# Kernel tuning notes

Measured on AMD Instinct MI355X. Metric: run time of the kernel, lower is better.

## Reference

```python
import jax, jax.numpy as jnp
import numpy as np

B, DIM, L, H, W = 4, 128, 256, 8, 8
N = L * H * W
D_INNER, D_STATE, D_CONV, DT_RANK = 128, 8, 4, 8


def _ln(x, w, b, eps=1e-5):
    m = x.mean(-1, keepdims=True)
    v = ((x - m) ** 2).mean(-1, keepdims=True)
    return (x - m) * jax.lax.rsqrt(v + eps) * w + b


def _mamba_fusion(x, z_in, p, i):
    # x, z_in: (B, N, DIM). x drives the SSM; z_in provides the cross-modal gate.
    u = x @ p['Wx'][i]                                    # (B, N, D_INNER)
    z = z_in @ p['Wz'][i]                                 # (B, N, D_INNER)
    # causal depthwise conv1d along tokens, kernel D_CONV (torch pad=k-1 then truncate)
    up = jnp.pad(u, ((0, 0), (D_CONV - 1, 0), (0, 0)))
    w = p['conv_w'][i]                                    # (D_INNER, D_CONV)
    uc = sum(up[:, k:k + u.shape[1], :] * w[:, k] for k in range(D_CONV)) + p['conv_b'][i]
    uc = jax.nn.silu(uc)
    x_dbl = uc @ p['Wxproj'][i]                           # (B, N, DT_RANK + 2*D_STATE)
    dt_r, Bm, Cm = jnp.split(x_dbl, [DT_RANK, DT_RANK + D_STATE], axis=-1)
    dt = jax.nn.softplus(dt_r @ p['Wdt'][i] + p['bdt'][i])  # (B, N, D_INNER)
    A = -jnp.exp(p['A_log'][i])                           # (D_INNER, D_STATE)
    dA = jnp.exp(dt[..., None] * A)                       # (B, N, D_INNER, D_STATE)
    dBu = dt[..., None] * Bm[:, :, None, :] * uc[..., None]

    def step(h, inp):
        dA_t, dBu_t, C_t = inp
        h = dA_t * h + dBu_t                              # (B, D_INNER, D_STATE)
        return h, jnp.einsum('bds,bs->bd', h, C_t)

    h0 = jnp.zeros((u.shape[0], D_INNER, D_STATE), u.dtype)
    _, ys = jax.lax.scan(step, h0, (dA.swapaxes(0, 1), dBu.swapaxes(0, 1), Cm.swapaxes(0, 1)))
    y = ys.swapaxes(0, 1) + p['Dp'][i] * uc
    y = y * jax.nn.silu(z)
    return y @ p['Wout_m'][i] + p['bout_m'][i]


def _cross_block(in0, in1, p, i):
    skip = in0
    a = _ln(in0, p['ln0_w'][i], p['ln0_b'][i])
    b = _ln(in1, p['ln1_w'][i], p['ln1_b'][i])
    return skip + _mamba_fusion(a, b, p, i)


def setup_inputs() -> dict:
    key = jax.random.key(0)
    ks = jax.random.split(key, 16)
    s_in = 1.0 / np.sqrt(DIM)
    s_di = 1.0 / np.sqrt(D_INNER)
    inp = {
        'front': jax.random.normal(ks[0], (B, DIM, L, H, W), jnp.float32),
        'back': jax.random.normal(ks[1], (B, DIM, L, H, W), jnp.float32),
        'ln0_w': jnp.ones((2, DIM), jnp.float32),
        'ln0_b': jnp.zeros((2, DIM), jnp.float32),
        'ln1_w': jnp.ones((2, DIM), jnp.float32),
        'ln1_b': jnp.zeros((2, DIM), jnp.float32),
        'Wx': jax.random.normal(ks[2], (2, DIM, D_INNER), jnp.float32) * s_in,
        'Wz': jax.random.normal(ks[3], (2, DIM, D_INNER), jnp.float32) * s_in,
        'conv_w': jax.random.normal(ks[4], (2, D_INNER, D_CONV), jnp.float32) * 0.5,
        'conv_b': jnp.zeros((2, D_INNER), jnp.float32),
        'Wxproj': jax.random.normal(ks[5], (2, D_INNER, DT_RANK + 2 * D_STATE), jnp.float32) * s_di,
        'Wdt': jax.random.normal(ks[6], (2, DT_RANK, D_INNER), jnp.float32) * (1.0 / np.sqrt(DT_RANK)),
        'bdt': jnp.full((2, D_INNER), -4.6, jnp.float32),  # softplus^-1(~0.01)
        'A_log': jnp.broadcast_to(jnp.log(jnp.arange(1, D_STATE + 1, dtype=jnp.float32)), (2, D_INNER, D_STATE)).copy(),
        'Dp': jnp.ones((2, D_INNER), jnp.float32),
        'Wout_m': jax.random.normal(ks[7], (2, D_INNER, DIM), jnp.float32) * s_di,
        'bout_m': jnp.zeros((2, DIM), jnp.float32),
        'Wout': jax.random.normal(ks[8], (DIM, DIM), jnp.float32) * s_in,
        'bout': jnp.zeros((DIM,), jnp.float32),
    }
    return inp


def reference(front, back, ln0_w, ln0_b, ln1_w, ln1_b, Wx, Wz, conv_w, conv_b,
              Wxproj, Wdt, bdt, A_log, Dp, Wout_m, bout_m, Wout, bout):
    p = dict(ln0_w=ln0_w, ln0_b=ln0_b, ln1_w=ln1_w, ln1_b=ln1_b, Wx=Wx, Wz=Wz,
             conv_w=conv_w, conv_b=conv_b, Wxproj=Wxproj, Wdt=Wdt, bdt=bdt,
             A_log=A_log, Dp=Dp, Wout_m=Wout_m, bout_m=bout_m)
    ff = front.reshape(B, DIM, N).swapaxes(1, 2)          # (B, N, DIM)
    bf = back.reshape(B, DIM, N).swapaxes(1, 2)
    f_fus = _cross_block(ff, bf, p, 0)
    b_fus = _cross_block(bf, ff, p, 1)
    fusion = ((f_fus + b_fus) * 0.5) @ Wout + bout
    return fusion.swapaxes(1, 2).reshape(B, DIM, L, H, W)
```

## Files before the change

### kernel.cpp

```cpp
#include <hip/hip_runtime.h>

#define DEV static __device__ __forceinline__

typedef short s16x8 __attribute__((ext_vector_type(8)));
typedef float f32x4 __attribute__((ext_vector_type(4)));
typedef unsigned short u16;

DEV float b2f(u16 u){ return __uint_as_float(((unsigned int)u) << 16); }
DEV u16 f2b(float f){
  unsigned int x = __float_as_uint(f);
  x += 0x7fffu + ((x >> 16) & 1u);
  return (u16)(x >> 16);
}
DEV float silu_f(float x){ return x * __builtin_amdgcn_rcpf(1.f + __expf(-x)); }
DEV float softplus_f(float x){ return (x > 15.f) ? x : __logf(1.f + __expf(x)); }
DEV bool detf32(const void* lnw){ return *(const unsigned int*)lnw == 0x3F800000u; }
DEV float ldin(const void* p, long long i, bool f){
  return f ? ((const float*)p)[i] : b2f(((const u16*)p)[i]);
}

static constexpr int BATCH = 4;
static constexpr int NSEQ  = 16384;
static constexpr int RTOT  = BATCH * NSEQ;
static constexpr int GCH   = 256;
static constexpr int DIRSZ = BATCH*GCH*128*8;

DEV int swz(int row, int col){ return (row << 7) + (col ^ ((row & 7) << 3)); }

__global__ __launch_bounds__(256) void k_setup(
                        const void* ln0w, const void* ln0b, const void* ln1w, const void* ln1b,
                        const void* Wx, const void* Wz, const void* Wxp, const void* Wdt,
                        const void* bdt, const void* Alog, const void* convw, const void* convb,
                        const void* Dpr, const void* Woutm, const void* boutm,
                        const void* Wout, const void* bout,
                        u16* Wuz, u16* WdtBC, u16* Wcat, u16* WoutT,
                        float* buz, float* bdtf, float* bcat, float* boutf,
                        float* Aexp, float* convwF, float* convbF, float* DpF)
{
  bool f = detf32(ln0w);
  int tid = blockIdx.x * 256 + threadIdx.x;
  int gs  = gridDim.x * 256;
  for (int idx = tid; idx < 2*256*128; idx += gs){
    int d = idx >> 15; int n = (idx >> 7) & 255; int k = idx & 127;
    float wv;
    if (n < 128) wv = ldin(ln0w, d*128+k, f) * ldin(Wx, (long long)(d*128+k)*128 + n, f);
    else         wv = ldin(ln1w, (1-d)*128+k, f) * ldin(Wz, (long long)((1-d)*128+k)*128 + (n-128), f);
    Wuz[idx] = f2b(wv);
  }
  for (int idx = tid; idx < 2*256; idx += gs){
    int d = idx >> 8; int n = idx & 255;
    float s = 0.f;
    if (n < 128){
      for (int k = 0; k < 128; ++k)
        s += ldin(ln0b, d*128+k, f) * ldin(Wx, (long long)(d*128+k)*128 + n, f);
    } else {
      for (int k = 0; k < 128; ++k)
        s += ldin(ln1b, (1-d)*128+k, f) * ldin(Wz, (long long)((1-d)*128+k)*128 + (n-128), f);
    }
    buz[idx] = s;
  }
  for (int idx = tid; idx < 2*128; idx += gs)
    bdtf[idx] = ldin(bdt, idx, f);
  for (int idx = tid; idx < 2*144*128; idx += gs){
    int i = idx / (144*128); int rem = idx % (144*128); int n = rem >> 7; int k = rem & 127;
    if (n < 128){
      float s = 0.f;
      for (int j = 0; j < 8; ++j)
        s += ldin(Wxp, (long long)(i*128+k)*24 + j, f) * ldin(Wdt, (long long)(i*8+j)*128 + n, f);
      WdtBC[idx] = f2b(s);
    } else {
      WdtBC[idx] = f2b(ldin(Wxp, (long long)(i*128+k)*24 + (n - 120), f));
    }
  }
  for (int idx = tid; idx < 128*256; idx += gs){
    int n = idx >> 8; int k = idx & 255;
    Wcat[idx] = f2b(ldin(Woutm, (long long)k*128 + n, f));
  }
  for (int idx = tid; idx < 128*128; idx += gs){
    int n = idx >> 7, k = idx & 127;
    WoutT[idx] = f2b(ldin(Wout, (long long)k*128 + n, f));
  }
  for (int idx = tid; idx < 128; idx += gs){
    bcat[idx]  = ldin(boutm, idx, f) + ldin(boutm, 128 + idx, f);
    boutf[idx] = ldin(bout, idx, f);
  }
  for (int idx = tid; idx < 2*128*8; idx += gs)
    Aexp[idx] = -expf(ldin(Alog, idx, f));
  for (int idx = tid; idx < 2*128*4; idx += gs)
    convwF[idx] = ldin(convw, idx, f);
  for (int idx = tid; idx < 2*128; idx += gs){
    convbF[idx] = ldin(convb, idx, f);
    DpF[idx]   = ldin(Dpr, idx, f);
  }
}

__global__ __launch_bounds__(256) void k_ln(const void* front, const void* back, const void* ln0w,
                                            u16* xf, u16* xb, u16* sfbh)
{
  bool fF = detf32(ln0w);
  __shared__ u16 Af[64][130];
  __shared__ u16 Ab[64][130];
  __shared__ float Mf[64], Rf[64], Mb[64], Rb[64];
  int tid = threadIdx.x;
  long long r0 = (long long)blockIdx.x * 64;
  int b  = (int)(r0 >> 14);
  int n0 = (int)(r0 & 16383);
  if (fF){
    const float* fp = (const float*)front;
    const float* bp = (const float*)back;
    for (int it = 0; it < 8; ++it){
      int d = it*16 + (tid >> 4);
      int t = (tid & 15) * 4;
      long long gi = ((long long)(b*128 + d))*NSEQ + n0 + t;
      float4 vf = *(const float4*)&fp[gi];
      float4 vb = *(const float4*)&bp[gi];
      Af[t+0][d] = f2b(vf.x); Af[t+1][d] = f2b(vf.y);
      Af[t+2][d] = f2b(vf.z); Af[t+3][d] = f2b(vf.w);
      Ab[t+0][d] = f2b(vb.x); Ab[t+1][d] = f2b(vb.y);
      Ab[t+2][d] = f2b(vb.z); Ab[t+3][d] = f2b(vb.w);
    }
  } else {
    const u16* fp = (const u16*)front;
    const u16* bp = (const u16*)back;
    for (int it = 0; it < 4; ++it){
      int d = it*32 + (tid >> 3);
      int t = (tid & 7) * 8;
      long long gi = ((long long)(b*128 + d))*NSEQ + n0 + t;
      uint4 vf = *(const uint4*)&fp[gi];
      uint4 vb = *(const uint4*)&bp[gi];
      Af[t+0][d] = (u16)vf.x; Af[t+1][d] = (u16)(vf.x>>16);
      Af[t+2][d] = (u16)vf.y; Af[t+3][d] = (u16)(vf.y>>16);
      Af[t+4][d] = (u16)vf.z; Af[t+5][d] = (u16)(vf.z>>16);
      Af[t+6][d] = (u16)vf.w; Af[t+7][d] = (u16)(vf.w>>16);
      Ab[t+0][d] = (u16)vb.x; Ab[t+1][d] = (u16)(vb.x>>16);
      Ab[t+2][d] = (u16)vb.y; Ab[t+3][d] = (u16)(vb.y>>16);
      Ab[t+4][d] = (u16)vb.z; Ab[t+5][d] = (u16)(vb.z>>16);
      Ab[t+6][d] = (u16)vb.w; Ab[t+7][d] = (u16)(vb.w>>16);
    }
  }
  __syncthreads();
  {
    int t = tid >> 2, sub = tid & 3;
    float s = 0.f, ss = 0.f, s2 = 0.f, ss2 = 0.f;
    for (int k = 0; k < 32; ++k){
      float v = b2f(Af[t][sub*32 + k]); s  += v; ss  += v*v;
      float w = b2f(Ab[t][sub*32 + k]); s2 += w; ss2 += w*w;
    }
    for (int m = 1; m < 4; m <<= 1){
      s  += __shfl_xor(s,  m, 64); ss  += __shfl_xor(ss,  m, 64);
      s2 += __shfl_xor(s2, m, 64); ss2 += __shfl_xor(ss2, m, 64);
    }
    if (sub == 0){
      float mf = s  * (1.f/128.f); float vf = ss  * (1.f/128.f) - mf*mf;
      Mf[t] = mf; Rf[t] = rsqrtf(vf + 1e-5f);
      float mb = s2 * (1.f/128.f); float vb = ss2 * (1.f/128.f) - mb*mb;
      Mb[t] = mb; Rb[t] = rsqrtf(vb + 1e-5f);
    }
  }
  __syncthreads();
  for (int it = 0; it < 8; ++it){
    int t = it*8 + (tid >> 5);
    int c = (tid & 31) * 4;
    float mf = Mf[t], rf = Rf[t], mb = Mb[t], rb = Rb[t];
    float f0 = b2f(Af[t][c+0]), f1 = b2f(Af[t][c+1]), f2 = b2f(Af[t][c+2]), f3 = b2f(Af[t][c+3]);
    float g0 = b2f(Ab[t][c+0]), g1 = b2f(Ab[t][c+1]), g2 = b2f(Ab[t][c+2]), g3 = b2f(Ab[t][c+3]);
    ushort4 xo, zo, so;
    xo.x = f2b((f0-mf)*rf); xo.y = f2b((f1-mf)*rf); xo.z = f2b((f2-mf)*rf); xo.w = f2b((f3-mf)*rf);
    zo.x = f2b((g0-mb)*rb); zo.y = f2b((g1-mb)*rb); zo.z = f2b((g2-mb)*rb); zo.w = f2b((g3-mb)*rb);
    so.x = f2b(f0+g0); so.y = f2b(f1+g1); so.z = f2b(f2+g2); so.w = f2b(f3+g3);
    long long o = (r0 + t)*128 + c;
    *(ushort4*)&xf[o] = xo;
    *(ushort4*)&xb[o] = zo;
    *(ushort4*)&sfbh[o] = so;
  }
}

__global__ __launch_bounds__(256) void k_guz(const u16* __restrict__ xf,
                                             const u16* __restrict__ xb,
                                             const u16* __restrict__ Wuz,
                                             const float* __restrict__ buz,
                                             u16* __restrict__ u0, u16* __restrict__ u1,
                                             u16* __restrict__ z0, u16* __restrict__ z1)
{
  int dir = blockIdx.y;
  const u16* A = dir ? xb : xf;
  const u16* Wt = Wuz + dir*256*128;
  const float* bias = buz + dir*256;
  u16* outU = dir ? u1 : u0;
  u16* outZ = dir ? z0 : z1;
  __shared__ u16 Wl[256][72];
  __shared__ u16 Al[64][72];
  int tid = threadIdx.x;
  long long r0 = (long long)blockIdx.x * 64;
  int w = tid >> 6, lane = tid & 63;
  int q = lane >> 4, m = lane & 15;
  f32x4 acc[16];
  #pragma unroll
  for (int ct = 0; ct < 16; ++ct) acc[ct] = (f32x4){0.f,0.f,0.f,0.f};
  for (int kp = 0; kp < 2; ++kp){
    if (kp) __syncthreads();
    for (int ci = tid; ci < 256*8; ci += 256){
      int n = ci >> 3, c8 = ci & 7;
      *(uint4*)&Wl[n][c8*8] = *(const uint4*)&Wt[n*128 + kp*64 + c8*8];
    }
    for (int ci = tid; ci < 64*8; ci += 256){
      int rl = ci >> 3, c8 = ci & 7;
      *(uint4*)&Al[rl][c8*8] = *(const uint4*)&A[(r0 + rl)*128 + kp*64 + c8*8];
    }
    __syncthreads();
    #pragma unroll
    for (int kt = 0; kt < 2; ++kt){
      s16x8 af = *(const s16x8*)&Al[w*16 + m][kt*32 + q*8];
      #pragma unroll
      for (int ct = 0; ct < 16; ++ct){
        s16x8 bf = *(const s16x8*)&Wl[ct*16 + m][kt*32 + q*8];
        acc[ct] = __builtin_amdgcn_mfma_f32_16x16x32_bf16(af, bf, acc[ct], 0, 0, 0);
      }
    }
  }
  #pragma unroll
  for (int ct = 0; ct < 16; ++ct){
    int col = ct*16 + m;
    #pragma unroll
    for (int i = 0; i < 4; ++i){
      long long r = r0 + w*16 + q*4 + i;
      float v = acc[ct][i] + bias[col];
      if (col < 128) outU[r*128 + col] = f2b(v);
      else           outZ[r*128 + (col - 128)] = f2b(silu_f(v));
    }
  }
}

__global__ __launch_bounds__(256, 3) void k_cps(const u16* __restrict__ u0p,
                                             const u16* __restrict__ u1p,
                                             const float* __restrict__ convwF,
                                             const float* __restrict__ convbF,
                                             const u16* __restrict__ WdtBC,
                                             const float* __restrict__ bdtf,
                                             const float* __restrict__ Aexp,
                                             u16* __restrict__ uc0p, u16* __restrict__ uc1p,
                                             u16* __restrict__ yg,
                                             float* __restrict__ BCg,
                                             float* __restrict__ P, float* __restrict__ Q)
{
  __shared__ __align__(16) u16 AlF[64*128];
  __shared__ __align__(16) u16 WlF[144*128];
  int dir = blockIdx.y;
  const u16* u = dir ? u1p : u0p;
  u16* ucb = dir ? uc1p : uc0p;
  const u16* Wt = WdtBC + dir*18432;
  const float* bias = bdtf + dir*128;
  u16* dtb = yg + dir*128;
  float* BC = BCg + (long long)dir*RTOT*16;
  int tid = threadIdx.x;
  long long r0 = (long long)blockIdx.x * 64;
  int b  = (int)(r0 >> 14);
  int n0 = (int)(r0 & 16383);
  for (int ci = tid; ci < 144*16; ci += 256){
    int n = ci >> 4, c8 = ci & 15;
    *(uint4*)&WlF[(n << 7) + ((c8 ^ (n & 7)) << 3)] = *(const uint4*)&Wt[n*128 + c8*8];
  }
  {
    int c = tid & 127, h = tid >> 7;
    const float* wp = &convwF[(dir*128 + c)*4];
    float w0 = wp[0], w1 = wp[1], w2 = wp[2], w3 = wp[3];
    float cb = convbF[dir*128 + c];
    int t0 = h*32;
    const u16* up = u + (long long)b*NSEQ*128 + c;
    int nbase = n0 + t0;
    float win0 = (nbase-3 >= 0) ? b2f(up[(long long)(nbase-3)*128]) : 0.f;
    float win1 = (nbase-2 >= 0) ? b2f(up[(long long)(nbase-2)*128]) : 0.f;
    float win2 = (nbase-1 >= 0) ? b2f(up[(long long)(nbase-1)*128]) : 0.f;
    #pragma unroll
    for (int t = 0; t < 32; ++t){
      float cur = b2f(up[(long long)(nbase + t)*128]);
      float a = win0*w0 + win1*w1 + win2*w2 + cur*w3 + cb;
      u16 s = f2b(silu_f(a));
      AlF[swz(t0 + t, c)] = s;
      ucb[(r0 + t0 + t)*128 + c] = s;
      win0 = win1; win1 = win2; win2 = cur;
    }
  }
  __syncthreads();
  int w = tid >> 6, lane = tid & 63;
  int q = lane >> 4, m = lane & 15;
  f32x4 acc[9];
  #pragma unroll
  for (int ct = 0; ct < 9; ++ct) acc[ct] = (f32x4){0.f,0.f,0.f,0.f};
  #pragma unroll
  for (int kt = 0; kt < 4; ++kt){
    int sc = (kt*32 + q*8) ^ ((m & 7) << 3);
    s16x8 af = *(const s16x8*)&AlF[((w*16 + m) << 7) + sc];
    #pragma unroll
    for (int ct = 0; ct < 9; ++ct){
      s16x8 bf = *(const s16x8*)&WlF[((ct*16 + m) << 7) + sc];
      acc[ct] = __builtin_amdgcn_mfma_f32_16x16x32_bf16(af, bf, acc[ct], 0, 0, 0);
    }
  }
  __syncthreads();
  u16* Dl = WlF;
  float* BCl = (float*)&WlF[64*128];
  #pragma unroll
  for (int ct = 0; ct < 9; ++ct){
    int col = ct*16 + m;
    #pragma unroll
    for (int i = 0; i < 4; ++i){
      int rl = w*16 + q*4 + i;
      long long r = r0 + rl;
      float v = acc[ct][i];
      if (col < 128){
        u16 dv = f2b(softplus_f(v + bias[col]));
        dtb[r*256 + col] = dv;
        Dl[swz(rl, col)] = dv;
      } else {
        BC[r*16 + (col - 128)] = v;
        BCl[rl*16 + (col - 128)] = v;
      }
    }
  }
  __syncthreads();
  {
    int c = tid & 127, sh = tid >> 7;
    int g = (int)(r0 & 16383) >> 6;
    int base = sh*4;
    float Ac[4], Pr[4], H[4];
    bool fast = true;
    #pragma unroll
    for (int j = 0; j < 4; ++j){
      Ac[j] = Aexp[(dir*128 + c)*8 + base + j];
      fast = fast && (fabsf(Ac[j] + (float)(base + j + 1)) < 2e-4f);
      Pr[j] = 1.f; H[j] = 0.f;
    }
    if (fast){
      for (int t = 0; t < 64; ++t){
        int ce = swz(t, c);
        float d  = b2f(Dl[ce]);
        float uu = b2f(AlF[ce]);
        float du = d * uu;
        float E  = __expf(-d);
        float E2 = E*E, E3 = E2*E, E4 = E2*E2;
        float M  = base ? E4 : 1.f;
        float dA0 = M*E, dA1 = M*E2, dA2 = M*E3, dA3 = M*E4;
        H[0] = dA0*H[0] + du*BCl[t*16 + base+0]; Pr[0] *= dA0;
        H[1] = dA1*H[1] + du*BCl[t*16 + base+1]; Pr[1] *= dA1;
        H[2] = dA2*H[2] + du*BCl[t*16 + base+2]; Pr[2] *= dA2;
        H[3] = dA3*H[3] + du*BCl[t*16 + base+3]; Pr[3] *= dA3;
      }
    } else {
      for (int t = 0; t < 64; ++t){
        int ce = swz(t, c);
        float d  = b2f(Dl[ce]);
        float uu = b2f(AlF[ce]);
        float du = d * uu;
        #pragma unroll
        for (int j = 0; j < 4; ++j){
          float dA = __expf(d * Ac[j]);
          H[j]  = dA*H[j] + du*BCl[t*16 + base + j];
          Pr[j] *= dA;
        }
      }
    }
    long long o = (long long)dir*DIRSZ + (((long long)b*GCH + g)*128 + c)*8 + base;
    *(float4*)&P[o] = make_float4(Pr[0],Pr[1],Pr[2],Pr[3]);
    *(float4*)&Q[o] = make_float4(H[0],H[1],H[2],H[3]);
  }
}

__global__ __launch_bounds__(64) void k_scan2(const float* __restrict__ P,
                                              const float* __restrict__ Q,
                                              float* __restrict__ hinit)
{
  int idx = blockIdx.x*64 + threadIdx.x;
  int dir = idx >> 12;
  int rem = idx & 4095;
  int b  = rem >> 10;
  int cs = rem & 1023;
  long long base = (long long)dir*DIRSZ + (long long)b*GCH*1024 + cs;
  float h = 0.f;
  for (int g = 0; g < GCH; g += 8){
    long long o = base + (long long)g*1024;
    float p[8], qv[8];
    #pragma unroll
    for (int j = 0; j < 8; ++j){ p[j] = P[o + j*1024]; qv[j] = Q[o + j*1024]; }
    #pragma unroll
    for (int j = 0; j < 8; ++j){
      hinit[o + j*1024] = h;
      h = p[j]*h + qv[j];
    }
  }
}

__global__ __launch_bounds__(256) void k_scan3(const u16* __restrict__ uc0p,
                                               const u16* __restrict__ uc1p,
                                               const float* __restrict__ BCg,
                                               const float* __restrict__ hinit,
                                               const u16* __restrict__ z0p,
                                               const u16* __restrict__ z1p,
                                               const float* __restrict__ DpF,
                                               const float* __restrict__ Aexp,
                                               u16* yg)
{
  __shared__ float Bl[128][8];
  __shared__ float Cl[128][8];
  int dir = blockIdx.y;
  const u16* uc = dir ? uc1p : uc0p;
  const u16* zs = dir ? z1p : z0p;
  const float* BC = BCg + (long long)dir*RTOT*16;
  int tid = threadIdx.x;
  int gp = blockIdx.x & 127;
  int b  = blockIdx.x >> 7;
  long long tokbase = (long long)b*NSEQ + gp*128;
  for (int idx = tid; idx < 128*8; idx += 256){
    int row = idx >> 3, s = idx & 7;
    Bl[row][s] = BC[(tokbase + row)*16 + s];
    Cl[row][s] = BC[(tokbase + row)*16 + 8 + s];
  }
  __syncthreads();
  int c = tid & 127;
  int gh = tid >> 7;
  int g = gp*2 + gh;
  int doff = dir*128;
  float Ac[8], H[8];
  long long ho = (long long)dir*DIRSZ + (((long long)b*GCH + g)*128 + c)*8;
  float4 h0 = *(const float4*)&hinit[ho];
  float4 h1 = *(const float4*)&hinit[ho + 4];
  H[0]=h0.x; H[1]=h0.y; H[2]=h0.z; H[3]=h0.w;
  H[4]=h1.x; H[5]=h1.y; H[6]=h1.z; H[7]=h1.w;
  bool fast = true;
  #pragma unroll
  for (int s = 0; s < 8; ++s){
    Ac[s] = Aexp[(dir*128 + c)*8 + s];
    fast = fast && (fabsf(Ac[s] + (float)(s + 1)) < 2e-4f);
  }
  float dpc = DpF[dir*128 + c];
  long long rbase = (long long)b*NSEQ + g*64;
  if (fast){
    for (int t = 0; t < 64; ++t){
      long long r = rbase + t;
      float d  = b2f(yg[r*256 + doff + c]);
      float uu = b2f(uc[r*128 + c]);
      float du = d * uu;
      int rowl = gh*64 + t;
      float E  = __expf(-d);
      float E2 = E*E, E3 = E2*E, E4 = E2*E2;
      float dA[8] = {E, E2, E3, E4, E4*E, E4*E2, E4*E3, E4*E4};
      float y = 0.f;
      #pragma unroll
      for (int s = 0; s < 8; ++s){
        H[s] = dA[s]*H[s] + du*Bl[rowl][s];
        y += H[s]*Cl[rowl][s];
      }
      float zv = b2f(zs[r*128 + c]);
      yg[r*256 + doff + c] = f2b((y + dpc*uu) * zv);
    }
  } else {
    for (int t = 0; t < 64; ++t){
      long long r = rbase + t;
      float d  = b2f(yg[r*256 + doff + c]);
      float uu = b2f(uc[r*128 + c]);
      float du = d * uu;
      int rowl = gh*64 + t;
      float y = 0.f;
      #pragma unroll
      for (int s = 0; s < 8; ++s){
        float dA = __expf(d * Ac[s]);
        H[s] = dA*H[s] + du*Bl[rowl][s];
        y += H[s]*Cl[rowl][s];
      }
      float zv = b2f(zs[r*128 + c]);
      yg[r*256 + doff + c] = f2b((y + dpc*uu) * zv);
    }
  }
}

__global__ __launch_bounds__(256) void k_tail(const u16* __restrict__ yg,
                                              const u16* __restrict__ Wcat,
                                              const float* __restrict__ bcat,
                                              const u16* __restrict__ sfbh,
                                              const u16* __restrict__ WoutT,
                                              const float* __restrict__ boutf,
                                              void* outp, const void* dflag)
{
  __shared__ u16 Wl[128][136];
  __shared__ u16 Al[64][136];
  __shared__ u16 Sl[64][136];
  int tid = threadIdx.x;
  long long r0 = (long long)blockIdx.x * 64;
  int w = tid >> 6, lane = tid & 63;
  int q = lane >> 4, m = lane & 15;
  f32x4 acc[8];
  #pragma unroll
  for (int ct = 0; ct < 8; ++ct) acc[ct] = (f32x4){0.f,0.f,0.f,0.f};
  for (int kp = 0; kp < 2; ++kp){
    if (kp) __syncthreads();
    for (int ci = tid; ci < 128*16; ci += 256){
      int n = ci >> 4, c8 = ci & 15;
      *(uint4*)&Wl[n][c8*8] = *(const uint4*)&Wcat[n*256 + kp*128 + c8*8];
    }
    for (int ci = tid; ci < 64*16; ci += 256){
      int rl = ci >> 4, c8 = ci & 15;
      *(uint4*)&Al[rl][c8*8] = *(const uint4*)&yg[(r0 + rl)*256 + kp*128 + c8*8];
    }
    __syncthreads();
    #pragma unroll
    for (int kt = 0; kt < 4; ++kt){
      s16x8 af = *(const s16x8*)&Al[w*16 + m][kt*32 + q*8];
      #pragma unroll
      for (int ct = 0; ct < 8; ++ct){
        s16x8 bf = *(const s16x8*)&Wl[ct*16 + m][kt*32 + q*8];
        acc[ct] = __builtin_amdgcn_mfma_f32_16x16x32_bf16(af, bf, acc[ct], 0, 0, 0);
      }
    }
  }
  #pragma unroll
  for (int ct = 0; ct < 8; ++ct){
    int col = ct*16 + m;
    #pragma unroll
    for (int i = 0; i < 4; ++i){
      int rl = w*16 + q*4 + i;
      long long r = r0 + rl;
      Sl[rl][col] = f2b(acc[ct][i] + bcat[col] + b2f(sfbh[r*128 + col]));
    }
  }
  __syncthreads();
  for (int ci = tid; ci < 128*16; ci += 256){
    int n = ci >> 4, c8 = ci & 15;
    *(uint4*)&Wl[n][c8*8] = *(const uint4*)&WoutT[n*128 + c8*8];
  }
  __syncthreads();
  f32x4 acc2[8];
  #pragma unroll
  for (int ct = 0; ct < 8; ++ct) acc2[ct] = (f32x4){0.f,0.f,0.f,0.f};
  #pragma unroll
  for (int kt = 0; kt < 4; ++kt){
    s16x8 af = *(const s16x8*)&Sl[w*16 + m][kt*32 + q*8];
    #pragma unroll
    for (int ct = 0; ct < 8; ++ct){
      s16x8 bf = *(const s16x8*)&Wl[ct*16 + m][kt*32 + q*8];
      acc2[ct] = __builtin_amdgcn_mfma_f32_16x16x32_bf16(af, bf, acc2[ct], 0, 0, 0);
    }
  }
  u16* Tl = &Al[0][0];
  #pragma unroll
  for (int ct = 0; ct < 8; ++ct){
    int col = ct*16 + m;
    #pragma unroll
    for (int i = 0; i < 4; ++i){
      int rl = w*16 + q*4 + i;
      Tl[col*68 + rl] = f2b(0.5f*acc2[ct][i] + boutf[col]);
    }
  }
  __syncthreads();
  long long b = r0 >> 14; long long tok0 = r0 & 16383;
  bool fo = detf32(dflag);
  if (fo){
    float* of = (float*)outp;
    for (int idx = tid; idx < 128*16; idx += 256){
      int n = idx >> 4; int t0 = (idx & 15)*4;
      float4 v;
      v.x = b2f(Tl[n*68 + t0+0]); v.y = b2f(Tl[n*68 + t0+1]);
      v.z = b2f(Tl[n*68 + t0+2]); v.w = b2f(Tl[n*68 + t0+3]);
      *(float4*)&of[(((long long)(b*128 + n)) << 14) + tok0 + t0] = v;
    }
  } else {
    u16* ob = (u16*)outp;
    for (int idx = tid; idx < 128*16; idx += 256){
      int n = idx >> 4; int t0 = (idx & 15)*4;
      ushort4 v;
      v.x = Tl[n*68 + t0+0]; v.y = Tl[n*68 + t0+1];
      v.z = Tl[n*68 + t0+2]; v.w = Tl[n*68 + t0+3];
      *(ushort4*)&ob[(((long long)(b*128 + n)) << 14) + tok0 + t0] = v;
    }
  }
}

extern "C" void kernel_launch(void* const* d_in, const int* in_sizes, int n_in,
                              void* d_out, int out_size, void* d_ws, size_t ws_size,
                              hipStream_t stream)
{
  (void)in_sizes; (void)n_in; (void)out_size; (void)ws_size;
  const void* front = d_in[0];
  const void* back  = d_in[1];
  const void* ln0w  = d_in[2];
  const void* ln0b  = d_in[3];
  const void* ln1w  = d_in[4];
  const void* ln1b  = d_in[5];
  const void* Wx    = d_in[6];
  const void* Wz    = d_in[7];
  const void* convw = d_in[8];
  const void* convb = d_in[9];
  const void* Wxp   = d_in[10];
  const void* Wdt   = d_in[11];
  const void* bdt   = d_in[12];
  const void* Alog  = d_in[13];
  const void* Dpr   = d_in[14];
  const void* Woutm = d_in[15];
  const void* boutm = d_in[16];
  const void* Wout  = d_in[17];
  const void* bout  = d_in[18];

  char* p = (char*)d_ws;
  auto alloc = [&](size_t bytes) -> void* {
    void* q = (void*)p; p += (bytes + 255) & ~(size_t)255; return q;
  };
  u16*   xf    = (u16*)  alloc((size_t)RTOT*128*2);
  u16*   xb    = (u16*)  alloc((size_t)RTOT*128*2);
  u16*   sfbh  = (u16*)  alloc((size_t)RTOT*128*2);
  u16*   u0    = (u16*)  alloc((size_t)RTOT*128*2);
  u16*   u1    = (u16*)  alloc((size_t)RTOT*128*2);
  u16*   z0    = (u16*)  alloc((size_t)RTOT*128*2);
  u16*   z1    = (u16*)  alloc((size_t)RTOT*128*2);
  float* BC    = (float*)alloc((size_t)2*RTOT*16*4);
  float* Pb    = (float*)alloc((size_t)2*DIRSZ*4);
  float* Qb    = (float*)alloc((size_t)2*DIRSZ*4);
  float* hin   = (float*)alloc((size_t)2*DIRSZ*4);
  u16*   yg    = (u16*)  alloc((size_t)RTOT*256*2);
  u16*   Wuz   = (u16*)  alloc(2*256*128*2);
  u16*   WdtBC = (u16*)  alloc(2*144*128*2);
  u16*   Wcat  = (u16*)  alloc(128*256*2);
  u16*   WoutT = (u16*)  alloc(128*128*2);
  float* buz   = (float*)alloc(2*256*4);
  float* bdtf  = (float*)alloc(2*128*4);
  float* bcat  = (float*)alloc(128*4);
  float* boutf = (float*)alloc(128*4);
  float* Aexp  = (float*)alloc(2*128*8*4);
  float* convwF= (float*)alloc(2*128*4*4);
  float* convbF= (float*)alloc(2*128*4);
  float* DpF   = (float*)alloc(2*128*4);

  k_setup<<<128,256,0,stream>>>(ln0w,ln0b,ln1w,ln1b,Wx,Wz,Wxp,Wdt,bdt,Alog,convw,convb,Dpr,
                                Woutm,boutm,Wout,bout,
                                Wuz,WdtBC,Wcat,WoutT,buz,bdtf,bcat,boutf,Aexp,
                                convwF,convbF,DpF);
  k_ln<<<RTOT/64,256,0,stream>>>(front,back,ln0w,xf,xb,sfbh);

  dim3 g2(RTOT/64, 2);
  k_guz<<<g2,256,0,stream>>>(xf, xb, Wuz, buz, u0, u1, z0, z1);
  k_cps<<<g2,256,0,stream>>>(u0, u1, convwF, convbF, WdtBC, bdtf, Aexp,
                             xf, xb, yg, BC, Pb, Qb);
  k_scan2<<<128,64,0,stream>>>(Pb, Qb, hin);
  dim3 g3(BATCH*GCH/2, 2);
  k_scan3<<<g3,256,0,stream>>>(xf, xb, BC, hin, z0, z1, DpF, Aexp, yg);
  k_tail<<<RTOT/64,256,0,stream>>>(yg, Wcat, bcat, sfbh, WoutT, boutf, d_out, ln0w);
}
```

Measured before the change: 329.4 us.

## Swizzle k_guz LDS, simplify chunk-scan decay products, trim k_tail LDS

k_guz drops its padded shared tiles for XOR-swizzled 64-wide rows to avoid bank conflicts and asks for 4 blocks per CU. In the chunk scan, the running decay product is no longer multiplied every step. It is recomputed once from the sum of dt, the fast path splits by state half with vectorized B loads, and the generic path uses exp(sum*A). k_tail reuses the Al and Wl buffers instead of a third shared tile, which cuts LDS use so 3 blocks per CU can fit, at the cost of an extra barrier. The exp-of-sum form may differ slightly in rounding from the multiplied product.

```diff
diff --git a/kernel.cpp b/kernel.cpp
--- a/kernel.cpp
+++ b/kernel.cpp
@@ -175,7 +175,7 @@
   }
 }
 
-__global__ __launch_bounds__(256) void k_guz(const u16* __restrict__ xf,
+__global__ __launch_bounds__(256, 4) void k_guz(const u16* __restrict__ xf,
                                              const u16* __restrict__ xb,
                                              const u16* __restrict__ Wuz,
                                              const float* __restrict__ buz,
@@ -188,8 +188,8 @@
   const float* bias = buz + dir*256;
   u16* outU = dir ? u1 : u0;
   u16* outZ = dir ? z0 : z1;
-  __shared__ u16 Wl[256][72];
-  __shared__ u16 Al[64][72];
+  __shared__ __align__(16) u16 Wl[256*64];
+  __shared__ __align__(16) u16 Al[64*64];
   int tid = threadIdx.x;
   long long r0 = (long long)blockIdx.x * 64;
   int w = tid >> 6, lane = tid & 63;
@@ -201,19 +201,20 @@
     if (kp) __syncthreads();
     for (int ci = tid; ci < 256*8; ci += 256){
       int n = ci >> 3, c8 = ci & 7;
-      *(uint4*)&Wl[n][c8*8] = *(const uint4*)&Wt[n*128 + kp*64 + c8*8];
+      *(uint4*)&Wl[(n << 6) + ((c8 ^ (n & 7)) << 3)] = *(const uint4*)&Wt[n*128 + kp*64 + c8*8];
     }
     for (int ci = tid; ci < 64*8; ci += 256){
       int rl = ci >> 3, c8 = ci & 7;
-      *(uint4*)&Al[rl][c8*8] = *(const uint4*)&A[(r0 + rl)*128 + kp*64 + c8*8];
+      *(uint4*)&Al[(rl << 6) + ((c8 ^ (rl & 7)) << 3)] = *(const uint4*)&A[(r0 + rl)*128 + kp*64 + c8*8];
     }
     __syncthreads();
     #pragma unroll
     for (int kt = 0; kt < 2; ++kt){
-      s16x8 af = *(const s16x8*)&Al[w*16 + m][kt*32 + q*8];
+      int sc = ((kt*4 + q) ^ (m & 7)) << 3;
+      s16x8 af = *(const s16x8*)&Al[((w*16 + m) << 6) + sc];
       #pragma unroll
       for (int ct = 0; ct < 16; ++ct){
-        s16x8 bf = *(const s16x8*)&Wl[ct*16 + m][kt*32 + q*8];
+        s16x8 bf = *(const s16x8*)&Wl[((ct*16 + m) << 6) + sc];
         acc[ct] = __builtin_amdgcn_mfma_f32_16x16x32_bf16(af, bf, acc[ct], 0, 0, 0);
       }
     }
@@ -329,22 +330,46 @@
     for (int j = 0; j < 4; ++j){
       Ac[j] = Aexp[(dir*128 + c)*8 + base + j];
       fast = fast && (fabsf(Ac[j] + (float)(base + j + 1)) < 2e-4f);
-      Pr[j] = 1.f; H[j] = 0.f;
-    }
+      H[j] = 0.f;
+    }
+    float sd = 0.f;
     if (fast){
-      for (int t = 0; t < 64; ++t){
-        int ce = swz(t, c);
-        float d  = b2f(Dl[ce]);
-        float uu = b2f(AlF[ce]);
-        float du = d * uu;
-        float E  = __expf(-d);
-        float E2 = E*E, E3 = E2*E, E4 = E2*E2;
-        float M  = base ? E4 : 1.f;
-        float dA0 = M*E, dA1 = M*E2, dA2 = M*E3, dA3 = M*E4;
-        H[0] = dA0*H[0] + du*BCl[t*16 + base+0]; Pr[0] *= dA0;
-        H[1] = dA1*H[1] + du*BCl[t*16 + base+1]; Pr[1] *= dA1;
-        H[2] = dA2*H[2] + du*BCl[t*16 + base+2]; Pr[2] *= dA2;
-        H[3] = dA3*H[3] + du*BCl[t*16 + base+3]; Pr[3] *= dA3;
+      if (sh == 0){
+        for (int t = 0; t < 64; ++t){
+          int ce = swz(t, c);
+          float d  = b2f(Dl[ce]);
+          float uu = b2f(AlF[ce]);
+          float du = d * uu;
+          sd += d;
+          float E  = __expf(-d);
+          float E2 = E*E, E3 = E2*E, E4 = E2*E2;
+          float4 bc = *(const float4*)&BCl[t*16];
+          H[0] = E *H[0] + du*bc.x;
+          H[1] = E2*H[1] + du*bc.y;
+          H[2] = E3*H[2] + du*bc.z;
+          H[3] = E4*H[3] + du*bc.w;
+        }
+        float Es = __expf(-sd);
+        Pr[0] = Es; Pr[1] = Es*Es; Pr[2] = Pr[1]*Es; Pr[3] = Pr[1]*Pr[1];
+      } else {
+        for (int t = 0; t < 64; ++t){
+          int ce = swz(t, c);
+          float d  = b2f(Dl[ce]);
+          float uu = b2f(AlF[ce]);
+          float du = d * uu;
+          sd += d;
+          float E  = __expf(-d);
+          float E2 = E*E, E4 = E2*E2;
+          float E5 = E4*E, E6 = E5*E, E7 = E6*E, E8 = E7*E;
+          float4 bc = *(const float4*)&BCl[t*16 + 4];
+          H[0] = E5*H[0] + du*bc.x;
+          H[1] = E6*H[1] + du*bc.y;
+          H[2] = E7*H[2] + du*bc.z;
+          H[3] = E8*H[3] + du*bc.w;
+        }
+        float Es = __expf(-sd);
+        float Es2 = Es*Es, Es4 = Es2*Es2;
+        Pr[0] = Es4*Es; Pr[1] = Es4*Es2; Pr[2] = Pr[1]*Es; Pr[3] = Es4*Es4;
       }
     } else {
       for (int t = 0; t < 64; ++t){
@@ -352,13 +377,15 @@
         float d  = b2f(Dl[ce]);
         float uu = b2f(AlF[ce]);
         float du = d * uu;
+        sd += d;
         #pragma unroll
         for (int j = 0; j < 4; ++j){
           float dA = __expf(d * Ac[j]);
           H[j]  = dA*H[j] + du*BCl[t*16 + base + j];
-          Pr[j] *= dA;
         }
       }
+      #pragma unroll
+      for (int j = 0; j < 4; ++j) Pr[j] = __expf(sd * Ac[j]);
     }
     long long o = (long long)dir*DIRSZ + (((long long)b*GCH + g)*128 + c)*8 + base;
     *(float4*)&P[o] = make_float4(Pr[0],Pr[1],Pr[2],Pr[3]);
@@ -473,7 +500,7 @@
   }
 }
 
-__global__ __launch_bounds__(256) void k_tail(const u16* __restrict__ yg,
+__global__ __launch_bounds__(256, 3) void k_tail(const u16* __restrict__ yg,
                                               const u16* __restrict__ Wcat,
                                               const float* __restrict__ bcat,
                                               const u16* __restrict__ sfbh,
@@ -483,7 +510,6 @@
 {
   __shared__ u16 Wl[128][136];
   __shared__ u16 Al[64][136];
-  __shared__ u16 Sl[64][136];
   int tid = threadIdx.x;
   long long r0 = (long long)blockIdx.x * 64;
   int w = tid >> 6, lane = tid & 63;
@@ -512,6 +538,7 @@
       }
     }
   }
+  __syncthreads();
   #pragma unroll
   for (int ct = 0; ct < 8; ++ct){
     int col = ct*16 + m;
@@ -519,10 +546,9 @@
     for (int i = 0; i < 4; ++i){
       int rl = w*16 + q*4 + i;
       long long r = r0 + rl;
-      Sl[rl][col] = f2b(acc[ct][i] + bcat[col] + b2f(sfbh[r*128 + col]));
-    }
-  }
-  __syncthreads();
+      Al[rl][col] = f2b(acc[ct][i] + bcat[col] + b2f(sfbh[r*128 + col]));
+    }
+  }
   for (int ci = tid; ci < 128*16; ci += 256){
     int n = ci >> 4, c8 = ci & 15;
     *(uint4*)&Wl[n][c8*8] = *(const uint4*)&WoutT[n*128 + c8*8];
@@ -533,14 +559,15 @@
   for (int ct = 0; ct < 8; ++ct) acc2[ct] = (f32x4){0.f,0.f,0.f,0.f};
   #pragma unroll
   for (int kt = 0; kt < 4; ++kt){
-    s16x8 af = *(const s16x8*)&Sl[w*16 + m][kt*32 + q*8];
+    s16x8 af = *(const s16x8*)&Al[w*16 + m][kt*32 + q*8];
     #pragma unroll
     for (int ct = 0; ct < 8; ++ct){
       s16x8 bf = *(const s16x8*)&Wl[ct*16 + m][kt*32 + q*8];
       acc2[ct] = __builtin_amdgcn_mfma_f32_16x16x32_bf16(af, bf, acc2[ct], 0, 0, 0);
     }
   }
-  u16* Tl = &Al[0][0];
+  __syncthreads();
+  u16* Tl = &Wl[0][0];
   #pragma unroll
   for (int ct = 0; ct < 8; ++ct){
     int col = ct*16 + m;
```

After: 326.5 us. About the same (-0.9%).
